# Kernel optimization log

Measured on AMD Instinct MI355X. Metric: run time of the kernel, lower is better.

Reference implementation:

```python
import jax, jax.numpy as jnp
import numpy as np

T, K, D_SLOTS, D_IN, D_HID, EPSILON = 3, 11, 64, 128, 256, 1e-8


def _layer_norm(x, g, b, eps=1e-5):
    m = jnp.mean(x, axis=-1, keepdims=True)
    v = jnp.mean((x - m) ** 2, axis=-1, keepdims=True)
    return (x - m) * jax.lax.rsqrt(v + eps) * g + b


def _gru_cell(x, h, w_ih, w_hh, b_ih, b_hh):
    # torch.nn.GRUCell math; w_ih/w_hh stored as [D, 3D] (input-major)
    gx = x @ w_ih + b_ih
    gh = h @ w_hh + b_hh
    xr, xz, xn = jnp.split(gx, 3, axis=-1)
    hr, hz, hn = jnp.split(gh, 3, axis=-1)
    r = jax.nn.sigmoid(xr + hr)
    z = jax.nn.sigmoid(xz + hz)
    n = jnp.tanh(xn + r * hn)
    return (1.0 - z) * n + z * h


def setup_inputs() -> dict:
    key = jax.random.key(0)
    ks = jax.random.split(key, 12)
    B, N = 64, 4096
    s = 0.02
    return {
        "inputs": jax.random.normal(ks[0], (B, N, D_IN), jnp.float32),
        "ln_in_g": jnp.ones((D_IN,), jnp.float32),
        "ln_in_b": jnp.zeros((D_IN,), jnp.float32),
        "Wk": jax.random.normal(ks[1], (D_IN, D_SLOTS), jnp.float32) * s,
        "Wv": jax.random.normal(ks[2], (D_IN, D_SLOTS), jnp.float32) * s,
        "init_latents": jax.random.normal(ks[3], (1, K, D_SLOTS), jnp.float32),
        "ln_q_g": jnp.ones((D_SLOTS,), jnp.float32),
        "ln_q_b": jnp.zeros((D_SLOTS,), jnp.float32),
        "Wq": jax.random.normal(ks[4], (D_SLOTS, D_SLOTS), jnp.float32) * s,
        "w_ih": jax.random.normal(ks[5], (D_SLOTS, 3 * D_SLOTS), jnp.float32) * s,
        "w_hh": jax.random.normal(ks[6], (D_SLOTS, 3 * D_SLOTS), jnp.float32) * s,
        "b_ih": jnp.zeros((3 * D_SLOTS,), jnp.float32),
        "b_hh": jnp.zeros((3 * D_SLOTS,), jnp.float32),
        "ln_f_g": jnp.ones((D_SLOTS,), jnp.float32),
        "ln_f_b": jnp.zeros((D_SLOTS,), jnp.float32),
        "W1": jax.random.normal(ks[7], (D_SLOTS, D_HID), jnp.float32) * s,
        "b1": jnp.zeros((D_HID,), jnp.float32),
        "W2": jax.random.normal(ks[8], (D_HID, D_SLOTS), jnp.float32) * s,
        "b2": jnp.zeros((D_SLOTS,), jnp.float32),
    }


def reference(inputs, ln_in_g, ln_in_b, Wk, Wv, init_latents, ln_q_g, ln_q_b, Wq,
              w_ih, w_hh, b_ih, b_hh, ln_f_g, ln_f_b, W1, b1, W2, b2):
    B = inputs.shape[0]
    x = _layer_norm(inputs, ln_in_g, ln_in_b)          # [B,N,128]
    keys = x @ Wk                                       # [B,N,D]
    vals = x @ Wv                                       # [B,N,D]
    slots = jnp.broadcast_to(init_latents, (B, K, D_SLOTS))
    scale = D_SLOTS ** (-0.5)
    attn2 = None
    for _ in range(T):
        slots_prev = slots
        q = _layer_norm(slots, ln_q_g, ln_q_b) @ Wq     # [B,K,D]
        logits = scale * jnp.einsum('bnc,bmc->bnm', keys, q)  # [B,N,K]
        attn = jax.nn.softmax(logits, axis=-1) + EPSILON
        attn2 = attn
        attn_n = attn / jnp.sum(attn, axis=1, keepdims=True)   # competing norm over inputs
        updates = jnp.einsum('bnm,bnc->bmc', attn_n, vals)     # [B,K,D]
        slots = _gru_cell(updates.reshape(B * K, D_SLOTS),
                          slots_prev.reshape(B * K, D_SLOTS),
                          w_ih, w_hh, b_ih, b_hh).reshape(B, K, D_SLOTS)
        h = jax.nn.relu(_layer_norm(slots, ln_f_g, ln_f_b) @ W1 + b1)
        slots = slots + (h @ W2 + b2)
    return slots, attn2
```

## Files before the change

### kernel.cpp

```cpp
#include <hip/hip_runtime.h>

#define DIN   128
#define DSL   64
#define KSL   11
#define NTOK  4096
#define NB    64
#define NSPLIT 32
#define LN_EPS   1e-5f
#define ATTN_EPS 1e-8f
#define SCALE    0.125f

typedef __bf16 bf16x8 __attribute__((ext_vector_type(8)));
typedef float  f32x4  __attribute__((ext_vector_type(4)));
typedef unsigned int u32x4 __attribute__((ext_vector_type(4)));

static __device__ __forceinline__ bf16x8 ntload8(const __bf16* p) {
  union { u32x4 u; bf16x8 v; } c;
  c.u = __builtin_nontemporal_load((const u32x4*)p);
  return c.v;
}

__launch_bounds__(704)
__global__ void k_prepinit(const float* __restrict__ Wk, const float* __restrict__ Wv,
                           const float* __restrict__ g, const float* __restrict__ b,
                           __bf16* __restrict__ WTf, float* __restrict__ EP,
                           const float* __restrict__ init_lat, const float* __restrict__ qg,
                           const float* __restrict__ qb, const float* __restrict__ Wq,
                           float* __restrict__ slots, float* __restrict__ q) {
  const int blk = blockIdx.x, tid = threadIdx.x;
  if (blk < 8) {
    if (tid < 256) {
      const int t = blk * 256 + tid;
      const int fid = t >> 6, lane = t & 63;
      const int ks = fid >> 3, nt = fid & 7;
      const int col = nt * 16 + (lane & 15);
      const int kb  = ks * 32 + (lane >> 4) * 8;
      union { uint4 u; __bf16 h[8]; } o;
#pragma unroll
      for (int j = 0; j < 8; ++j) {
        const int k = kb + j;
        const float v = ((col < 64) ? Wk[k * 64 + col] : Wv[k * 64 + (col - 64)]) * g[k];
        o.h[j] = (__bf16)v;
      }
      *((uint4*)WTf + t) = o.u;
    }
    return;
  }
  if (blk == 8) {
    if (tid < 128) {
      const float* __restrict__ W = (tid < 64) ? Wk : Wv;
      const int cc = tid & 63;
      float G = 0.f, Bt = 0.f;
      for (int k = 0; k < 128; ++k) {
        const float w = W[k * 64 + cc];
        G += g[k] * w; Bt += b[k] * w;
      }
      EP[tid] = G; EP[128 + tid] = Bt;
    }
    return;
  }
  const int bb = blk - 9;
  const int k = tid >> 6, c = tid & 63;
  const float s = init_lat[k * DSL + c];
  slots[(size_t)(bb * KSL + k) * DSL + c] = s;
  float sum = s, sq = s * s;
#pragma unroll
  for (int o = 32; o > 0; o >>= 1) { sum += __shfl_xor(sum, o); sq += __shfl_xor(sq, o); }
  const float m = sum * (1.f / 64.f);
  const float rstd = rsqrtf(sq * (1.f / 64.f) - m * m + LN_EPS);
  const float qn = (s - m) * rstd * qg[c] + qb[c];
  float acc = 0.f;
  for (int i = 0; i < DSL; ++i) acc += __shfl(qn, i) * Wq[i * DSL + c];
  q[(size_t)(bb * KSL + k) * DSL + c] = acc * SCALE;
}

__launch_bounds__(256)
__global__ void k_lnproj(const float* __restrict__ inp, const __bf16* __restrict__ WTf,
                         const float* __restrict__ EP, __bf16* __restrict__ keys,
                         __bf16* __restrict__ valsT) {
  __shared__ __bf16 Xs[4][16][136];
  __shared__ float rowstats[4][16][2];
  const int tid = threadIdx.x, wave = tid >> 6, lane = tid & 63;
  const int half = lane >> 5, hl = lane & 31;
  const int t = lane & 15, g = lane >> 4;
  const int rbase = blockIdx.x * 64 + wave * 16;

  float4 xr[8];
#pragma unroll
  for (int p = 0; p < 8; ++p)
    xr[p] = *(const float4*)(inp + (size_t)(rbase + 2 * p + half) * DIN + hl * 4);

  float s[8], sq[8];
#pragma unroll
  for (int p = 0; p < 8; ++p) {
    s[p]  = xr[p].x + xr[p].y + xr[p].z + xr[p].w;
    sq[p] = xr[p].x * xr[p].x + xr[p].y * xr[p].y + xr[p].z * xr[p].z + xr[p].w * xr[p].w;
    union { ushort4 u; __bf16 h[4]; } pk;
    pk.h[0] = (__bf16)xr[p].x; pk.h[1] = (__bf16)xr[p].y;
    pk.h[2] = (__bf16)xr[p].z; pk.h[3] = (__bf16)xr[p].w;
    *(ushort4*)&Xs[wave][2 * p + half][hl * 4] = pk.u;
  }
#pragma unroll
  for (int o = 16; o > 0; o >>= 1) {
#pragma unroll
    for (int p = 0; p < 8; ++p) { s[p] += __shfl_xor(s[p], o); sq[p] += __shfl_xor(sq[p], o); }
  }
  if (hl < 8) {
    const int p = hl;
    const float m = s[p] * (1.f / 128.f);
    const float rstd = rsqrtf(sq[p] * (1.f / 128.f) - m * m + LN_EPS);
    rowstats[wave][2 * p + half][0] = m;
    rowstats[wave][2 * p + half][1] = rstd;
  }
  const bf16x8* __restrict__ Wv8 = (const bf16x8*)WTf;
  f32x4 acc[8] = {};
#pragma unroll
  for (int ks = 0; ks < 4; ++ks) {
    const bf16x8 xf = *(const bf16x8*)&Xs[wave][t][ks * 32 + g * 8];
#pragma unroll
    for (int nt = 0; nt < 8; ++nt) {
      const bf16x8 wf = Wv8[(ks * 8 + nt) * 64 + lane];
      acc[nt] = __builtin_amdgcn_mfma_f32_16x16x32_bf16(wf, xf, acc[nt], 0, 0, 0);
    }
  }
  const float2 mrs = *(const float2*)&rowstats[wave][t][0];
  const float rstd = mrs.y, mm = mrs.x * mrs.y;
  const int bidx = rbase >> 12;
  const int tIB  = (rbase & 4095) + t;
#pragma unroll
  for (int nt = 0; nt < 8; ++nt) {
    const float4 Gv = *(const float4*)(EP + nt * 16 + g * 4);
    const float4 Bv = *(const float4*)(EP + 128 + nt * 16 + g * 4);
    const float o0 = rstd * acc[nt][0] - mm * Gv.x + Bv.x;
    const float o1 = rstd * acc[nt][1] - mm * Gv.y + Bv.y;
    const float o2 = rstd * acc[nt][2] - mm * Gv.z + Bv.z;
    const float o3 = rstd * acc[nt][3] - mm * Gv.w + Bv.w;
    if (nt < 4) {
      union { unsigned long long u; __bf16 h[4]; } pk;
      pk.h[0] = (__bf16)o0; pk.h[1] = (__bf16)o1; pk.h[2] = (__bf16)o2; pk.h[3] = (__bf16)o3;
      *(unsigned long long*)&keys[(size_t)(rbase + t) * 64 + nt * 16 + g * 4] = pk.u;
    } else {
      const int vc = (nt - 4) * 16 + g * 4;
      valsT[((size_t)bidx * 64 + vc + 0) * NTOK + tIB] = (__bf16)o0;
      valsT[((size_t)bidx * 64 + vc + 1) * NTOK + tIB] = (__bf16)o1;
      valsT[((size_t)bidx * 64 + vc + 2) * NTOK + tIB] = (__bf16)o2;
      valsT[((size_t)bidx * 64 + vc + 3) * NTOK + tIB] = (__bf16)o3;
    }
  }
}

template <bool LAST>
__launch_bounds__(64)
__global__ void k_attn(const __bf16* __restrict__ keys, const __bf16* __restrict__ valsT,
                       const float* __restrict__ q, float* __restrict__ Upart,
                       float* __restrict__ Spart, float* __restrict__ attn_out) {
  __shared__ __bf16 P[2][16][72];
  const int b = blockIdx.x >> 5, sp = blockIdx.x & 31;
  const int lane = threadIdx.x;
  const int g = lane >> 4, t = lane & 15;

  bf16x8 qf[2];
#pragma unroll
  for (int ks = 0; ks < 2; ++ks) {
    float4 q0 = {0.f, 0.f, 0.f, 0.f}, q1 = {0.f, 0.f, 0.f, 0.f};
    if (t < KSL) {
      const float* __restrict__ qp = q + (size_t)(b * KSL + t) * DSL + ks * 32 + g * 8;
      q0 = *(const float4*)qp; q1 = *(const float4*)(qp + 4);
    }
    qf[ks][0] = (__bf16)q0.x; qf[ks][1] = (__bf16)q0.y;
    qf[ks][2] = (__bf16)q0.z; qf[ks][3] = (__bf16)q0.w;
    qf[ks][4] = (__bf16)q1.x; qf[ks][5] = (__bf16)q1.y;
    qf[ks][6] = (__bf16)q1.z; qf[ks][7] = (__bf16)q1.w;
  }

  const __bf16* __restrict__ kbase = keys + ((size_t)b * NTOK + sp * 128) * DSL;
  const __bf16* __restrict__ vbase = valsT + (size_t)b * DSL * NTOK + sp * 128;
  float sacc[4] = {0.f, 0.f, 0.f, 0.f};
  f32x4 U[4] = {};

#pragma unroll
  for (int gr = 0; gr < 2; ++gr) {
    const int tb = gr * 64;
    bf16x8 kf[4][2];
#pragma unroll
    for (int tile = 0; tile < 4; ++tile)
#pragma unroll
      for (int ks = 0; ks < 2; ++ks) {
        const __bf16* ap = kbase + (size_t)(tb + tile * 16 + t) * DSL + ks * 32 + g * 8;
        kf[tile][ks] = LAST ? ntload8(ap) : *(const bf16x8*)ap;
      }
    bf16x8 vf[2][4];
#pragma unroll
    for (int ks = 0; ks < 2; ++ks)
#pragma unroll
      for (int ct = 0; ct < 4; ++ct) {
        const __bf16* ap = vbase + (size_t)(ct * 16 + t) * NTOK + tb + ks * 32 + g * 8;
        vf[ks][ct] = LAST ? ntload8(ap) : *(const bf16x8*)ap;
      }
    f32x4 c[4] = {};
#pragma unroll
    for (int ks = 0; ks < 2; ++ks)
#pragma unroll
      for (int tile = 0; tile < 4; ++tile)
        c[tile] = __builtin_amdgcn_mfma_f32_16x16x32_bf16(qf[ks], kf[tile][ks], c[tile], 0, 0, 0);
    float lg[4][4], mx[4];
#pragma unroll
    for (int tile = 0; tile < 4; ++tile) {
#pragma unroll
      for (int r = 0; r < 4; ++r)
        lg[tile][r] = (4 * g + r < KSL) ? c[tile][r] : -1e30f;
      mx[tile] = fmaxf(fmaxf(lg[tile][0], lg[tile][1]), fmaxf(lg[tile][2], lg[tile][3]));
    }
#pragma unroll
    for (int tile = 0; tile < 4; ++tile) mx[tile] = fmaxf(mx[tile], __shfl_xor(mx[tile], 16));
#pragma unroll
    for (int tile = 0; tile < 4; ++tile) mx[tile] = fmaxf(mx[tile], __shfl_xor(mx[tile], 32));
    float se[4];
#pragma unroll
    for (int tile = 0; tile < 4; ++tile) {
#pragma unroll
      for (int r = 0; r < 4; ++r) lg[tile][r] = __expf(lg[tile][r] - mx[tile]);
      se[tile] = lg[tile][0] + lg[tile][1] + lg[tile][2] + lg[tile][3];
    }
#pragma unroll
    for (int tile = 0; tile < 4; ++tile) se[tile] += __shfl_xor(se[tile], 16);
#pragma unroll
    for (int tile = 0; tile < 4; ++tile) se[tile] += __shfl_xor(se[tile], 32);
#pragma unroll
    for (int tile = 0; tile < 4; ++tile) {
      const float inv = 1.f / se[tile];
#pragma unroll
      for (int r = 0; r < 4; ++r) {
        const float a = lg[tile][r] * inv + ATTN_EPS;
        sacc[r] += a;
        P[gr][4 * g + r][tile * 16 + t] = (__bf16)a;
        if constexpr (LAST) {
          if (4 * g + r < KSL)
            __builtin_nontemporal_store(
                a, &attn_out[((size_t)b * NTOK + sp * 128 + tb + tile * 16 + t) * KSL + 4 * g + r]);
        }
      }
    }
#pragma unroll
    for (int ks = 0; ks < 2; ++ks) {
      const bf16x8 pf = *(const bf16x8*)&P[gr][t][ks * 32 + g * 8];
#pragma unroll
      for (int ct = 0; ct < 4; ++ct)
        U[ct] = __builtin_amdgcn_mfma_f32_16x16x32_bf16(pf, vf[ks][ct], U[ct], 0, 0, 0);
    }
  }

  float* __restrict__ up = Upart + (size_t)(b * NSPLIT + sp) * (KSL * DSL);
#pragma unroll
  for (int ct = 0; ct < 4; ++ct)
#pragma unroll
    for (int r = 0; r < 4; ++r)
      if (4 * g + r < KSL) up[(4 * g + r) * DSL + ct * 16 + t] = U[ct][r];

#pragma unroll
  for (int r = 0; r < 4; ++r) {
#pragma unroll
    for (int o = 1; o < 16; o <<= 1) sacc[r] += __shfl_xor(sacc[r], o);
  }
  if (t == 0) {
    float* __restrict__ spp = Spart + (size_t)(b * NSPLIT + sp) * 16;
#pragma unroll
    for (int r = 0; r < 4; ++r) spp[4 * g + r] = sacc[r];
  }
}

template <bool LAST>
__launch_bounds__(128)
__global__ void k_update(const float* __restrict__ Upart, const float* __restrict__ Spart,
                         float* __restrict__ slots, const float* __restrict__ w_ih,
                         const float* __restrict__ w_hh, const float* __restrict__ b_ih,
                         const float* __restrict__ b_hh, const float* __restrict__ fg,
                         const float* __restrict__ fb, const float* __restrict__ W1,
                         const float* __restrict__ b1v, const float* __restrict__ W2,
                         const float* __restrict__ b2v, const float* __restrict__ qg,
                         const float* __restrict__ qbv, const float* __restrict__ Wq,
                         float* __restrict__ q, float* __restrict__ out_slots) {
  __shared__ float rU[2][64];
  __shared__ float rS[2];
  __shared__ float rG[2][6][64];
  __shared__ float rH[2][4][64];
  __shared__ float rO[2][64];
  __shared__ float rQ[2][64];
  const int w = threadIdx.x >> 6, c = threadIdx.x & 63;
  const int row = blockIdx.x;
  const int b = row / 11, k = row - b * 11;

  float upi = 0.f, ssp = 0.f;
  for (int s = w * 16; s < w * 16 + 16; ++s) {
    upi += __builtin_nontemporal_load(&Upart[((size_t)(b * NSPLIT + s) * KSL + k) * DSL + c]);
    ssp += __builtin_nontemporal_load(&Spart[(size_t)(b * NSPLIT + s) * 16 + k]);
  }
  rU[w][c] = upi;
  if (c == 0) rS[w] = ssp;
  const float h = slots[(size_t)row * DSL + c];
  __syncthreads();
  const float u = (rU[0][c] + rU[1][c]) / (rS[0] + rS[1]);

  float gr = 0.f, gz = 0.f, gn = 0.f, hr = 0.f, hz = 0.f, hn = 0.f;
  for (int i = w * 32; i < w * 32 + 32; ++i) {
    const float ui = __shfl(u, i), hi = __shfl(h, i);
    gr += ui * w_ih[i * 192 + c];       hr += hi * w_hh[i * 192 + c];
    gz += ui * w_ih[i * 192 + 64 + c];  hz += hi * w_hh[i * 192 + 64 + c];
    gn += ui * w_ih[i * 192 + 128 + c]; hn += hi * w_hh[i * 192 + 128 + c];
  }
  rG[w][0][c] = gr; rG[w][1][c] = gz; rG[w][2][c] = gn;
  rG[w][3][c] = hr; rG[w][4][c] = hz; rG[w][5][c] = hn;
  __syncthreads();
  gr = rG[0][0][c] + rG[1][0][c] + b_ih[c];
  gz = rG[0][1][c] + rG[1][1][c] + b_ih[64 + c];
  gn = rG[0][2][c] + rG[1][2][c] + b_ih[128 + c];
  hr = rG[0][3][c] + rG[1][3][c] + b_hh[c];
  hz = rG[0][4][c] + rG[1][4][c] + b_hh[64 + c];
  hn = rG[0][5][c] + rG[1][5][c] + b_hh[128 + c];
  const float r = 1.f / (1.f + __expf(-(gr + hr)));
  const float z = 1.f / (1.f + __expf(-(gz + hz)));
  const float nn = tanhf(gn + r * hn);
  float sv = (1.f - z) * nn + z * h;

  float sum = sv, sq = sv * sv;
#pragma unroll
  for (int o = 32; o > 0; o >>= 1) { sum += __shfl_xor(sum, o); sq += __shfl_xor(sq, o); }
  float m = sum * (1.f / 64.f);
  float rstd = rsqrtf(sq * (1.f / 64.f) - m * m + LN_EPS);
  const float sl = (sv - m) * rstd * fg[c] + fb[c];

  float h0 = 0.f, h1 = 0.f, h2 = 0.f, h3 = 0.f;
  for (int i = w * 32; i < w * 32 + 32; ++i) {
    const float si = __shfl(sl, i);
    h0 += si * W1[i * 256 + c];        h1 += si * W1[i * 256 + 64 + c];
    h2 += si * W1[i * 256 + 128 + c];  h3 += si * W1[i * 256 + 192 + c];
  }
  rH[w][0][c] = h0; rH[w][1][c] = h1; rH[w][2][c] = h2; rH[w][3][c] = h3;
  __syncthreads();
  h0 = fmaxf(rH[0][0][c] + rH[1][0][c] + b1v[c], 0.f);
  h1 = fmaxf(rH[0][1][c] + rH[1][1][c] + b1v[64 + c], 0.f);
  h2 = fmaxf(rH[0][2][c] + rH[1][2][c] + b1v[128 + c], 0.f);
  h3 = fmaxf(rH[0][3][c] + rH[1][3][c] + b1v[192 + c], 0.f);

  float o = 0.f;
  {
    const float ha = (w == 0) ? h0 : h2;
    const float hb = (w == 0) ? h1 : h3;
    const int base = w * 128;
    for (int j = 0; j < 64; ++j) o += __shfl(ha, j) * W2[(base + j) * DSL + c];
    for (int j = 0; j < 64; ++j) o += __shfl(hb, j) * W2[(base + 64 + j) * DSL + c];
  }
  rO[w][c] = o;
  __syncthreads();
  sv += rO[0][c] + rO[1][c] + b2v[c];

  if constexpr (LAST) {
    if (w == 0)
      __builtin_nontemporal_store(sv, &out_slots[(size_t)row * DSL + c]);
  } else {
    float s2 = sv, q2 = sv * sv;
#pragma unroll
    for (int o2 = 32; o2 > 0; o2 >>= 1) { s2 += __shfl_xor(s2, o2); q2 += __shfl_xor(q2, o2); }
    m = s2 * (1.f / 64.f);
    rstd = rsqrtf(q2 * (1.f / 64.f) - m * m + LN_EPS);
    const float qn = (sv - m) * rstd * qg[c] + qbv[c];
    float qa = 0.f;
    for (int i = w * 32; i < w * 32 + 32; ++i) qa += __shfl(qn, i) * Wq[i * DSL + c];
    rQ[w][c] = qa;
    __syncthreads();
    if (w == 0) {
      slots[(size_t)row * DSL + c] = sv;
      q[(size_t)row * DSL + c] = (rQ[0][c] + rQ[1][c]) * SCALE;
    }
  }
}

extern "C" void kernel_launch(void* const* d_in, const int* in_sizes, int n_in,
                              void* d_out, int out_size, void* d_ws, size_t ws_size,
                              hipStream_t stream) {
  const float* inp  = (const float*)d_in[0];
  const float* lng  = (const float*)d_in[1];
  const float* lnb  = (const float*)d_in[2];
  const float* Wk   = (const float*)d_in[3];
  const float* Wv   = (const float*)d_in[4];
  const float* init = (const float*)d_in[5];
  const float* qg   = (const float*)d_in[6];
  const float* qbb  = (const float*)d_in[7];
  const float* Wq   = (const float*)d_in[8];
  const float* wih  = (const float*)d_in[9];
  const float* whh  = (const float*)d_in[10];
  const float* bih  = (const float*)d_in[11];
  const float* bhh  = (const float*)d_in[12];
  const float* fg   = (const float*)d_in[13];
  const float* fb   = (const float*)d_in[14];
  const float* W1   = (const float*)d_in[15];
  const float* b1   = (const float*)d_in[16];
  const float* W2   = (const float*)d_in[17];
  const float* b2   = (const float*)d_in[18];

  char* wsb = (char*)d_ws;
  __bf16* keys  = (__bf16*)wsb;
  __bf16* valsT = keys + (size_t)NB * NTOK * DSL;
  __bf16* WTf   = valsT + (size_t)NB * DSL * NTOK;
  float*  EP    = (float*)(WTf + 16384);
  float* slots = EP + 256;
  float* q     = slots + NB * KSL * DSL;
  float* Upart = q + NB * KSL * DSL;
  float* Spart = Upart + (size_t)NB * NSPLIT * KSL * DSL;

  float* out_slots = (float*)d_out;
  float* out_attn  = (float*)d_out + NB * KSL * DSL;

  k_prepinit<<<73, 704, 0, stream>>>(Wk, Wv, lng, lnb, WTf, EP,
                                     init, qg, qbb, Wq, slots, q);
  k_lnproj<<<4096, 256, 0, stream>>>(inp, WTf, EP, keys, valsT);
  for (int t = 0; t < 3; ++t) {
    if (t < 2) {
      k_attn<false><<<NB * NSPLIT, 64, 0, stream>>>(keys, valsT, q, Upart, Spart, nullptr);
      k_update<false><<<NB * KSL, 128, 0, stream>>>(Upart, Spart, slots, wih, whh, bih, bhh,
                                                    fg, fb, W1, b1, W2, b2, qg, qbb, Wq, q,
                                                    nullptr);
    } else {
      k_attn<true><<<NB * NSPLIT, 64, 0, stream>>>(keys, valsT, q, Upart, Spart, out_attn);
      k_update<true><<<NB * KSL, 128, 0, stream>>>(Upart, Spart, slots, wih, whh, bih, bhh,
                                                   fg, fb, W1, b1, W2, b2, qg, qbb, Wq, q,
                                                   out_slots);
    }
  }
}
```

Baseline: 153.3 us.

## Fuse first-iteration attention into LN/projection kernel via shared-memory keys/values

The first slot-attention iteration's softmax and attention-weighted value reduction now run inside k_lnproj. Each block stages its 64 tokens' bf16 keys and values in shared memory and has wave 0 compute partial updates and attention sums. This removes one k_attn launch and its re-read of keys and values from global memory for iteration one. In exchange, k_lnproj uses more shared memory and adds a block barrier, and k_update must reduce 64 partials instead of 32 on that iteration.

```diff
diff --git a/kernel.cpp b/kernel.cpp
--- a/kernel.cpp
+++ b/kernel.cpp
@@ -5,7 +5,6 @@
 #define KSL   11
 #define NTOK  4096
 #define NB    64
-#define NSPLIT 32
 #define LN_EPS   1e-5f
 #define ATTN_EPS 1e-8f
 #define SCALE    0.125f
@@ -76,10 +75,14 @@
 
 __launch_bounds__(256)
 __global__ void k_lnproj(const float* __restrict__ inp, const __bf16* __restrict__ WTf,
-                         const float* __restrict__ EP, __bf16* __restrict__ keys,
-                         __bf16* __restrict__ valsT) {
+                         const float* __restrict__ EP, const float* __restrict__ q,
+                         __bf16* __restrict__ keys, __bf16* __restrict__ valsT,
+                         float* __restrict__ Upart, float* __restrict__ Spart) {
   __shared__ __bf16 Xs[4][16][136];
   __shared__ float rowstats[4][16][2];
+  __shared__ __bf16 Ks[64][72];
+  __shared__ __bf16 Vs[64][72];
+  __shared__ __bf16 P[16][72];
   const int tid = threadIdx.x, wave = tid >> 6, lane = tid & 63;
   const int half = lane >> 5, hl = lane & 31;
   const int t = lane & 15, g = lane >> 4;
@@ -127,6 +130,7 @@
   const float rstd = mrs.y, mm = mrs.x * mrs.y;
   const int bidx = rbase >> 12;
   const int tIB  = (rbase & 4095) + t;
+  const int ltok = wave * 16 + t;
 #pragma unroll
   for (int nt = 0; nt < 8; ++nt) {
     const float4 Gv = *(const float4*)(EP + nt * 16 + g * 4);
@@ -139,13 +143,104 @@
       union { unsigned long long u; __bf16 h[4]; } pk;
       pk.h[0] = (__bf16)o0; pk.h[1] = (__bf16)o1; pk.h[2] = (__bf16)o2; pk.h[3] = (__bf16)o3;
       *(unsigned long long*)&keys[(size_t)(rbase + t) * 64 + nt * 16 + g * 4] = pk.u;
+      *(unsigned long long*)&Ks[ltok][nt * 16 + g * 4] = pk.u;
     } else {
       const int vc = (nt - 4) * 16 + g * 4;
-      valsT[((size_t)bidx * 64 + vc + 0) * NTOK + tIB] = (__bf16)o0;
-      valsT[((size_t)bidx * 64 + vc + 1) * NTOK + tIB] = (__bf16)o1;
-      valsT[((size_t)bidx * 64 + vc + 2) * NTOK + tIB] = (__bf16)o2;
-      valsT[((size_t)bidx * 64 + vc + 3) * NTOK + tIB] = (__bf16)o3;
-    }
+      const __bf16 h0 = (__bf16)o0, h1 = (__bf16)o1, h2 = (__bf16)o2, h3 = (__bf16)o3;
+      valsT[((size_t)bidx * 64 + vc + 0) * NTOK + tIB] = h0;
+      valsT[((size_t)bidx * 64 + vc + 1) * NTOK + tIB] = h1;
+      valsT[((size_t)bidx * 64 + vc + 2) * NTOK + tIB] = h2;
+      valsT[((size_t)bidx * 64 + vc + 3) * NTOK + tIB] = h3;
+      Vs[vc + 0][ltok] = h0;
+      Vs[vc + 1][ltok] = h1;
+      Vs[vc + 2][ltok] = h2;
+      Vs[vc + 3][ltok] = h3;
+    }
+  }
+  __syncthreads();
+  if (wave != 0) return;
+
+  const int b = blockIdx.x >> 6, sp = blockIdx.x & 63;
+  bf16x8 qf[2];
+#pragma unroll
+  for (int ks = 0; ks < 2; ++ks) {
+    float4 q0 = {0.f, 0.f, 0.f, 0.f}, q1 = {0.f, 0.f, 0.f, 0.f};
+    if (t < KSL) {
+      const float* __restrict__ qp = q + (size_t)(b * KSL + t) * DSL + ks * 32 + g * 8;
+      q0 = *(const float4*)qp; q1 = *(const float4*)(qp + 4);
+    }
+    qf[ks][0] = (__bf16)q0.x; qf[ks][1] = (__bf16)q0.y;
+    qf[ks][2] = (__bf16)q0.z; qf[ks][3] = (__bf16)q0.w;
+    qf[ks][4] = (__bf16)q1.x; qf[ks][5] = (__bf16)q1.y;
+    qf[ks][6] = (__bf16)q1.z; qf[ks][7] = (__bf16)q1.w;
+  }
+  f32x4 c[4] = {};
+#pragma unroll
+  for (int ks = 0; ks < 2; ++ks)
+#pragma unroll
+    for (int tile = 0; tile < 4; ++tile) {
+      const bf16x8 kf = *(const bf16x8*)&Ks[tile * 16 + t][ks * 32 + g * 8];
+      c[tile] = __builtin_amdgcn_mfma_f32_16x16x32_bf16(qf[ks], kf, c[tile], 0, 0, 0);
+    }
+  float lg[4][4], mx[4];
+#pragma unroll
+  for (int tile = 0; tile < 4; ++tile) {
+#pragma unroll
+    for (int r = 0; r < 4; ++r)
+      lg[tile][r] = (4 * g + r < KSL) ? c[tile][r] : -1e30f;
+    mx[tile] = fmaxf(fmaxf(lg[tile][0], lg[tile][1]), fmaxf(lg[tile][2], lg[tile][3]));
+  }
+#pragma unroll
+  for (int tile = 0; tile < 4; ++tile) mx[tile] = fmaxf(mx[tile], __shfl_xor(mx[tile], 16));
+#pragma unroll
+  for (int tile = 0; tile < 4; ++tile) mx[tile] = fmaxf(mx[tile], __shfl_xor(mx[tile], 32));
+  float se[4];
+#pragma unroll
+  for (int tile = 0; tile < 4; ++tile) {
+#pragma unroll
+    for (int r = 0; r < 4; ++r) lg[tile][r] = __expf(lg[tile][r] - mx[tile]);
+    se[tile] = lg[tile][0] + lg[tile][1] + lg[tile][2] + lg[tile][3];
+  }
+#pragma unroll
+  for (int tile = 0; tile < 4; ++tile) se[tile] += __shfl_xor(se[tile], 16);
+#pragma unroll
+  for (int tile = 0; tile < 4; ++tile) se[tile] += __shfl_xor(se[tile], 32);
+  float sacc[4] = {0.f, 0.f, 0.f, 0.f};
+#pragma unroll
+  for (int tile = 0; tile < 4; ++tile) {
+    const float inv = 1.f / se[tile];
+#pragma unroll
+    for (int r = 0; r < 4; ++r) {
+      const float a = lg[tile][r] * inv + ATTN_EPS;
+      sacc[r] += a;
+      P[4 * g + r][tile * 16 + t] = (__bf16)a;
+    }
+  }
+  f32x4 U[4] = {};
+#pragma unroll
+  for (int ks = 0; ks < 2; ++ks) {
+    const bf16x8 pf = *(const bf16x8*)&P[t][ks * 32 + g * 8];
+#pragma unroll
+    for (int ct = 0; ct < 4; ++ct) {
+      const bf16x8 vf = *(const bf16x8*)&Vs[ct * 16 + t][ks * 32 + g * 8];
+      U[ct] = __builtin_amdgcn_mfma_f32_16x16x32_bf16(pf, vf, U[ct], 0, 0, 0);
+    }
+  }
+  float* __restrict__ up = Upart + (size_t)(b * 64 + sp) * (KSL * DSL);
+#pragma unroll
+  for (int ct = 0; ct < 4; ++ct)
+#pragma unroll
+    for (int r = 0; r < 4; ++r)
+      if (4 * g + r < KSL) up[(4 * g + r) * DSL + ct * 16 + t] = U[ct][r];
+#pragma unroll
+  for (int r = 0; r < 4; ++r) {
+#pragma unroll
+    for (int o = 1; o < 16; o <<= 1) sacc[r] += __shfl_xor(sacc[r], o);
+  }
+  if (t == 0) {
+    float* __restrict__ spp = Spart + (size_t)(b * 64 + sp) * 16;
+#pragma unroll
+    for (int r = 0; r < 4; ++r) spp[4 * g + r] = sacc[r];
   }
 }
 
@@ -250,7 +345,7 @@
     }
   }
 
-  float* __restrict__ up = Upart + (size_t)(b * NSPLIT + sp) * (KSL * DSL);
+  float* __restrict__ up = Upart + (size_t)(b * 32 + sp) * (KSL * DSL);
 #pragma unroll
   for (int ct = 0; ct < 4; ++ct)
 #pragma unroll
@@ -263,13 +358,13 @@
     for (int o = 1; o < 16; o <<= 1) sacc[r] += __shfl_xor(sacc[r], o);
   }
   if (t == 0) {
-    float* __restrict__ spp = Spart + (size_t)(b * NSPLIT + sp) * 16;
+    float* __restrict__ spp = Spart + (size_t)(b * 32 + sp) * 16;
 #pragma unroll
     for (int r = 0; r < 4; ++r) spp[4 * g + r] = sacc[r];
   }
 }
 
-template <bool LAST>
+template <int NS, bool LAST>
 __launch_bounds__(128)
 __global__ void k_update(const float* __restrict__ Upart, const float* __restrict__ Spart,
                          float* __restrict__ slots, const float* __restrict__ w_ih,
@@ -291,9 +386,9 @@
   const int b = row / 11, k = row - b * 11;
 
   float upi = 0.f, ssp = 0.f;
-  for (int s = w * 16; s < w * 16 + 16; ++s) {
-    upi += __builtin_nontemporal_load(&Upart[((size_t)(b * NSPLIT + s) * KSL + k) * DSL + c]);
-    ssp += __builtin_nontemporal_load(&Spart[(size_t)(b * NSPLIT + s) * 16 + k]);
+  for (int s = w * (NS / 2); s < (w + 1) * (NS / 2); ++s) {
+    upi += __builtin_nontemporal_load(&Upart[((size_t)(b * NS + s) * KSL + k) * DSL + c]);
+    ssp += __builtin_nontemporal_load(&Spart[(size_t)(b * NS + s) * 16 + k]);
   }
   rU[w][c] = upi;
   if (c == 0) rS[w] = ssp;
@@ -406,25 +501,23 @@
   float* slots = EP + 256;
   float* q     = slots + NB * KSL * DSL;
   float* Upart = q + NB * KSL * DSL;
-  float* Spart = Upart + (size_t)NB * NSPLIT * KSL * DSL;
+  float* Spart = Upart + (size_t)NB * 64 * KSL * DSL;
 
   float* out_slots = (float*)d_out;
   float* out_attn  = (float*)d_out + NB * KSL * DSL;
 
   k_prepinit<<<73, 704, 0, stream>>>(Wk, Wv, lng, lnb, WTf, EP,
                                      init, qg, qbb, Wq, slots, q);
-  k_lnproj<<<4096, 256, 0, stream>>>(inp, WTf, EP, keys, valsT);
-  for (int t = 0; t < 3; ++t) {
-    if (t < 2) {
-      k_attn<false><<<NB * NSPLIT, 64, 0, stream>>>(keys, valsT, q, Upart, Spart, nullptr);
-      k_update<false><<<NB * KSL, 128, 0, stream>>>(Upart, Spart, slots, wih, whh, bih, bhh,
+  k_lnproj<<<4096, 256, 0, stream>>>(inp, WTf, EP, q, keys, valsT, Upart, Spart);
+  k_update<64, false><<<NB * KSL, 128, 0, stream>>>(Upart, Spart, slots, wih, whh, bih, bhh,
                                                     fg, fb, W1, b1, W2, b2, qg, qbb, Wq, q,
                                                     nullptr);
-    } else {
-      k_attn<true><<<NB * NSPLIT, 64, 0, stream>>>(keys, valsT, q, Upart, Spart, out_attn);
-      k_update<true><<<NB * KSL, 128, 0, stream>>>(Upart, Spart, slots, wih, whh, bih, bhh,
+  k_attn<false><<<NB * 32, 64, 0, stream>>>(keys, valsT, q, Upart, Spart, nullptr);
+  k_update<32, false><<<NB * KSL, 128, 0, stream>>>(Upart, Spart, slots, wih, whh, bih, bhh,
+                                                    fg, fb, W1, b1, W2, b2, qg, qbb, Wq, q,
+                                                    nullptr);
+  k_attn<true><<<NB * 32, 64, 0, stream>>>(keys, valsT, q, Upart, Spart, out_attn);
+  k_update<32, true><<<NB * KSL, 128, 0, stream>>>(Upart, Spart, slots, wih, whh, bih, bhh,
                                                    fg, fb, W1, b1, W2, b2, qg, qbb, Wq, q,
                                                    out_slots);
-    }
-  }
 }
```

After: 179.2 us. +16.9%, slower.
